# Kernel optimization log

Measured on AMD Instinct MI355X. Metric: run time of the kernel, lower is better.

## Reference

```python
import jax, jax.numpy as jnp
import numpy as np

B, C, HZ, HX = 32, 256, 13, 25

# ---------- basic layers ----------

def _conv1x1(x, w, b):
    # x: [B,Cin,H,W], w: [Cout,Cin]
    return jnp.einsum('bchw,oc->bohw', x, w) + b[None, :, None, None]

def _conv2d(x, w, b, pad):
    y = jax.lax.conv_general_dilated(x, w, (1, 1), [(pad, pad), (pad, pad)],
                                     dimension_numbers=('NCHW', 'OIHW', 'NCHW'))
    return y + b[None, :, None, None]

def _bn(x, gamma, beta, mean, var):
    # eval-mode batchnorm with running stats, eps=1e-5 (torch default)
    s = gamma / jnp.sqrt(var + 1e-5)
    return x * s[None, :, None, None] + (beta - mean * s)[None, :, None, None]

def _gelu(x):
    return jax.nn.gelu(x, approximate=False)  # torch nn.GELU default = exact erf

# ---------- sparsemax (softThresholdingOperation) ----------
# The torch topk version recursively refines unresolved rows with 2*topk; since
# 2*128>=169 and 2*512>=625 it is mathematically exact sparsemax here.

def _sparsemax_impl(s):
    s = s - jnp.max(s, axis=-1, keepdims=True)
    d = s.shape[-1]
    z = -jnp.sort(-s, axis=-1)                      # descending sort
    cs = jnp.cumsum(z, axis=-1) - 1.0
    k = jnp.arange(1, d + 1, dtype=s.dtype)
    support = k * z > cs
    supp = jnp.sum(support, axis=-1, keepdims=True)  # int support size
    tau = jnp.take_along_axis(cs, supp - 1, axis=-1) / supp.astype(s.dtype)
    out = jnp.maximum(s - tau, 0.0)
    return out, (out, supp)

@jax.custom_vjp
def sparsemax(s):
    return _sparsemax_impl(s)[0]

def _sm_fwd(s):
    return _sparsemax_impl(s)

def _sm_bwd(res, g):
    out, supp = res
    gi = jnp.where(out != 0, g, 0.0)
    v_hat = jnp.sum(gi, axis=-1, keepdims=True) / supp.astype(out.dtype)
    return (jnp.where(out != 0, gi - v_hat, gi),)

sparsemax.defvjp(_sm_fwd, _sm_bwd)

# ---------- connected components + fill holes (GPU-native, no scipy) ----------

def _dilate8_max(lab):
    # 3x3 max-pool label propagation (8-connectivity, matches np.ones((3,3)))
    Bb, H, W = lab.shape
    p = jnp.pad(lab, ((0, 0), (1, 1), (1, 1)))
    shifts = [p[:, i:i + H, j:j + W] for i in range(3) for j in range(3)]
    return jnp.max(jnp.stack(shifts, 0), 0)

def _dilate4_or(x):
    # cross-shaped binary dilation (4-connectivity, scipy fill_holes default)
    Bb, H, W = x.shape
    p = jnp.pad(x, ((0, 0), (1, 1), (1, 1)))
    return (p[:, 1:H + 1, 1:W + 1] | p[:, 0:H, 1:W + 1] | p[:, 2:H + 2, 1:W + 1]
            | p[:, 1:H + 1, 0:W] | p[:, 1:H + 1, 2:W + 2])

def _largest_cc_filled(m):
    # m: bool [B,H,W] -> float mask of largest 8-connected component, holes filled
    Bb, H, W = m.shape
    HW = H * W
    idx = jnp.arange(1, HW + 1, dtype=jnp.int32).reshape(1, H, W)
    lab0 = jnp.where(m, idx, 0)

    def body(st):
        lab, _ = st
        return (jnp.where(m, _dilate8_max(lab), 0), lab)

    lab = jax.lax.while_loop(lambda st: jnp.any(st[0] != st[1]), body,
                             (lab0, -jnp.ones_like(lab0)))[0]

    counts = jax.vmap(lambda l, mm: jnp.zeros(HW + 1, jnp.int32)
                      .at[l.ravel()].add(mm.ravel()))(lab, m.astype(jnp.int32))
    largest = jnp.argmax(counts.at[:, 0].set(-1), axis=-1).astype(jnp.int32)
    comp = (lab == largest[:, None, None]) & m

    # fill holes: flood-fill background (4-conn) from the border, invert
    bg = ~comp
    border = jnp.zeros((H, W), bool).at[0].set(True).at[-1].set(True) \
        .at[:, 0].set(True).at[:, -1].set(True)
    seed = bg & border[None]

    def body2(st):
        r, _ = st
        return (bg & _dilate4_or(r), r)

    reach = jax.lax.while_loop(lambda st: jnp.any(st[0] != st[1]), body2,
                               (seed, jnp.zeros_like(seed)))[0]
    return ~reach

# ---------- module forward ----------

def _forward(zf, xf, sup_w, sup_b, sup_gamma, sup_beta, sup_mean, sup_var,
             q_w, q_b, q_gamma, q_beta, q_mean, q_var,
             g_w1, g_b1, g_w2, g_b2, g_gamma, g_beta, g_mean, g_var,
             fi_w, fi_b, fi_gamma, fi_beta, fi_mean, fi_var,
             fi1_w, fi1_b, fi1_gamma, fi1_beta, fi1_mean, fi1_var):
    Bb, Cc, Hz, Wz = zf.shape
    _, _, Hx, Wx = xf.shape

    xf_trans = _gelu(_bn(_conv1x1(xf, q_w, q_b), q_gamma, q_beta, q_mean, q_var))
    zf_trans = _gelu(_bn(_conv1x1(zf, sup_w, sup_b), sup_gamma, sup_beta, sup_mean, sup_var))
    xf_g = _gelu(_bn(_conv1x1(_conv2d(xf, g_w1, g_b1, 1), g_w2, g_b2),
                     g_gamma, g_beta, g_mean, g_var))

    zt = zf_trans.reshape(Bb, Cc, Hz * Wz)
    xt = xf_trans.reshape(Bb, Cc, Hx * Wx)
    zp = zf.reshape(Bb, Cc, Hz * Wz)
    xp = xf.reshape(Bb, Cc, Hx * Wx)

    zf_s = sparsemax(jnp.einsum('bcn,bcm->bnm', zt, zt))      # [B,169,169]
    zp = zp + jnp.einsum('bcn,bnm->bcm', zp, zf_s)

    si = sparsemax(jnp.einsum('bcn,bcm->bnm', zp, xp))         # [B,169,625]
    si2 = sparsemax(jnp.einsum('bcn,bcm->bnm', zp, xt))
    si = si + si2

    mask2 = jax.lax.stop_gradient(jnp.mean(si2, axis=1)) != 0  # [B,625]
    mask = _largest_cc_filled(mask2.reshape(Bb, Hx, Wx)).astype(xf.dtype)[:, None]

    si_img = si.reshape(Bb, Hz * Wz, Hx, Wx)                   # [B,169,25,25]
    fi_out = _gelu(_bn(_conv1x1(si_img, fi_w, fi_b), fi_gamma, fi_beta, fi_mean, fi_var))
    concat = jnp.concatenate([fi_out, xf_g * mask], axis=1)
    return _gelu(_bn(_conv2d(concat, fi1_w, fi1_b, 2),
                     fi1_gamma, fi1_beta, fi1_mean, fi1_var))

# ---------- setup ----------

def setup_inputs() -> dict:
    key = jax.random.key(0)
    ks = jax.random.split(key, 40)
    f32 = jnp.float32

    def n(k, shape, s=0.05):
        return (jax.random.normal(k, shape) * s).astype(f32)

    inp = {}
    inp['zf'] = jax.random.normal(ks[0], (B, C, HZ, HZ), f32)
    inp['xf'] = jax.random.normal(ks[1], (B, C, HX, HX), f32)

    def bn_params(pfx, k0):
        inp[pfx + '_gamma'] = (1.0 + n(ks[k0], (C,))).astype(f32)
        inp[pfx + '_beta'] = n(ks[k0 + 1], (C,))
        inp[pfx + '_mean'] = n(ks[k0 + 2], (C,))
        inp[pfx + '_var'] = jax.random.uniform(ks[k0 + 3], (C,), f32, 0.5, 1.5)

    inp['sup_w'] = n(ks[2], (C, C), 0.06); inp['sup_b'] = n(ks[3], (C,))
    bn_params('sup', 4)
    inp['q_w'] = n(ks[8], (C, C), 0.06); inp['q_b'] = n(ks[9], (C,))
    bn_params('q', 10)
    inp['g_w1'] = n(ks[14], (C, C, 3, 3), 0.02); inp['g_b1'] = n(ks[15], (C,))
    inp['g_w2'] = n(ks[16], (C, C), 0.06); inp['g_b2'] = n(ks[17], (C,))
    bn_params('g', 18)
    inp['fi_w'] = n(ks[22], (C, HZ * HZ), 0.08); inp['fi_b'] = n(ks[23], (C,))
    bn_params('fi', 24)
    inp['fi1_w'] = n(ks[28], (C, 2 * C, 5, 5), 0.01); inp['fi1_b'] = n(ks[29], (C,))
    bn_params('fi1', 30)
    return inp


def reference(zf, xf, sup_w, sup_b, sup_gamma, sup_beta, sup_mean, sup_var,
              q_w, q_b, q_gamma, q_beta, q_mean, q_var,
              g_w1, g_b1, g_w2, g_b2, g_gamma, g_beta, g_mean, g_var,
              fi_w, fi_b, fi_gamma, fi_beta, fi_mean, fi_var,
              fi1_w, fi1_b, fi1_gamma, fi1_beta, fi1_mean, fi1_var):
    return _forward(zf, xf, sup_w, sup_b, sup_gamma, sup_beta, sup_mean, sup_var,
                    q_w, q_b, q_gamma, q_beta, q_mean, q_var,
                    g_w1, g_b1, g_w2, g_b2, g_gamma, g_beta, g_mean, g_var,
                    fi_w, fi_b, fi_gamma, fi_beta, fi_mean, fi_var,
                    fi1_w, fi1_b, fi1_gamma, fi1_beta, fi1_mean, fi1_var)
```

## Files before the change

kernel.cpp:

```cpp
#include <hip/hip_runtime.h>
#include <hip/hip_bf16.h>
#include <math.h>

#define BB  32
#define CC  256
#define NZ  169
#define NX  625

typedef _Float16 f16x4 __attribute__((ext_vector_type(4)));
typedef _Float16 f16x8 __attribute__((ext_vector_type(8)));
typedef float    f32x4 __attribute__((ext_vector_type(4)));

__device__ __forceinline__ float geluf(float x) {
  return 0.5f * x * (1.0f + erff(x * 0.7071067811865476f));
}

struct GP {
  const float* A;  const float* B;
  const float* bias; const float* gamma; const float* beta; const float* mean; const float* var;
  const float* resid;
  float* out;
  int M, N, K;
  long aB, bB, outB;
};

#define TM 64
#define TN 64
#define TK 16

template<int AG, int EPI>
__global__ __launch_bounds__(256) void gemm_k(GP p) {
  const int b  = blockIdx.z;
  const int m0 = blockIdx.y * TM;
  const int n0 = blockIdx.x * TN;
  const float* Ab = p.A + (size_t)b * p.aB;
  const float* Bb = p.B + (size_t)b * p.bB;
  __shared__ __align__(16) float As[TK][TM + 4];
  __shared__ __align__(16) float Bs[TK][TN + 4];
  const int tid = threadIdx.x;
  const int tx = tid & 15, ty = tid >> 4;
  float acc[4][4] = {{0.f}};
  const int nK = (p.K + TK - 1) / TK;
  for (int kb = 0; kb < nK; ++kb) {
    const int k0 = kb * TK;
    if (AG == 0) {
      #pragma unroll
      for (int i = 0; i < 4; ++i) {
        int e = tid * 4 + i;
        int am = e >> 4, ak = e & 15;
        int gm = m0 + am, gk = k0 + ak;
        float v = 0.f;
        if (gm < p.M && gk < p.K) v = Ab[(size_t)gm * p.K + gk];
        As[ak][am] = v;
      }
    } else {
      #pragma unroll
      for (int i = 0; i < 4; ++i) {
        int e = tid + 256 * i;
        int ak = e >> 6, am = e & 63;
        int gm = m0 + am, gk = k0 + ak;
        float v = 0.f;
        if (gm < p.M && gk < p.K) v = Ab[(size_t)gk * p.M + gm];
        As[ak][am] = v;
      }
    }
    #pragma unroll
    for (int i = 0; i < 4; ++i) {
      int e = tid + 256 * i;
      int bk = e >> 6, bn = e & 63;
      int gk = k0 + bk, gn = n0 + bn;
      float v = 0.f;
      if (gk < p.K && gn < p.N) v = Bb[(size_t)gk * p.N + gn];
      Bs[bk][bn] = v;
    }
    __syncthreads();
    #pragma unroll
    for (int kk = 0; kk < TK; ++kk) {
      float av[4], bv[4];
      #pragma unroll
      for (int i2 = 0; i2 < 4; ++i2) av[i2] = As[kk][ty * 4 + i2];
      #pragma unroll
      for (int j2 = 0; j2 < 4; ++j2) bv[j2] = Bs[kk][tx * 4 + j2];
      #pragma unroll
      for (int i2 = 0; i2 < 4; ++i2)
        #pragma unroll
        for (int j2 = 0; j2 < 4; ++j2)
          acc[i2][j2] = fmaf(av[i2], bv[j2], acc[i2][j2]);
    }
    __syncthreads();
  }
  #pragma unroll
  for (int i = 0; i < 4; ++i) {
    int gm = m0 + ty * 4 + i;
    if (gm >= p.M) continue;
    float bs = 0.f, sBN = 1.f, tBN = 0.f;
    if (EPI == 2) {
      bs = p.bias[gm];
      float sc = p.gamma[gm] / sqrtf(p.var[gm] + 1e-5f);
      sBN = sc; tBN = p.beta[gm] - p.mean[gm] * sc;
    }
    #pragma unroll
    for (int j = 0; j < 4; ++j) {
      int gn = n0 + tx * 4 + j;
      if (gn >= p.N) continue;
      float v = acc[i][j];
      if (EPI == 2) { v += bs; v = v * sBN + tBN; v = geluf(v); }
      if (EPI == 3) v += p.resid[(size_t)b * p.outB + (size_t)gm * p.N + gn];
      p.out[(size_t)b * p.outB + (size_t)gm * p.N + gn] = v;
    }
  }
}

struct GP2 {
  const float* A; const float* B1; const float* B2;
  float* out1; float* out2;
  int M, N, K;
  long aB, bB, outB;
};

__global__ __launch_bounds__(256) void gemm2_k(GP2 p) {
  const int b  = blockIdx.z;
  const int m0 = blockIdx.y * TM;
  const int n0 = blockIdx.x * TN;
  const float* Ab  = p.A  + (size_t)b * p.aB;
  const float* B1b = p.B1 + (size_t)b * p.bB;
  const float* B2b = p.B2 + (size_t)b * p.bB;
  __shared__ __align__(16) float As [TK][TM + 4];
  __shared__ __align__(16) float Bs1[TK][TN + 4];
  __shared__ __align__(16) float Bs2[TK][TN + 4];
  const int tid = threadIdx.x;
  const int tx = tid & 15, ty = tid >> 4;
  float acc1[4][4] = {{0.f}};
  float acc2[4][4] = {{0.f}};
  const int nK = (p.K + TK - 1) / TK;
  for (int kb = 0; kb < nK; ++kb) {
    const int k0 = kb * TK;
    #pragma unroll
    for (int i = 0; i < 4; ++i) {
      int e = tid + 256 * i;
      int ak = e >> 6, am = e & 63;
      int gm = m0 + am, gk = k0 + ak;
      float v = 0.f;
      if (gm < p.M && gk < p.K) v = Ab[(size_t)gk * p.M + gm];
      As[ak][am] = v;
    }
    #pragma unroll
    for (int i = 0; i < 4; ++i) {
      int e = tid + 256 * i;
      int bk = e >> 6, bn = e & 63;
      int gk = k0 + bk, gn = n0 + bn;
      float v1 = 0.f, v2 = 0.f;
      if (gk < p.K && gn < p.N) {
        v1 = B1b[(size_t)gk * p.N + gn];
        v2 = B2b[(size_t)gk * p.N + gn];
      }
      Bs1[bk][bn] = v1;
      Bs2[bk][bn] = v2;
    }
    __syncthreads();
    #pragma unroll
    for (int kk = 0; kk < TK; ++kk) {
      float av[4], bv1[4], bv2[4];
      #pragma unroll
      for (int i2 = 0; i2 < 4; ++i2) av[i2] = As[kk][ty * 4 + i2];
      #pragma unroll
      for (int j2 = 0; j2 < 4; ++j2) { bv1[j2] = Bs1[kk][tx * 4 + j2]; bv2[j2] = Bs2[kk][tx * 4 + j2]; }
      #pragma unroll
      for (int i2 = 0; i2 < 4; ++i2)
        #pragma unroll
        for (int j2 = 0; j2 < 4; ++j2) {
          acc1[i2][j2] = fmaf(av[i2], bv1[j2], acc1[i2][j2]);
          acc2[i2][j2] = fmaf(av[i2], bv2[j2], acc2[i2][j2]);
        }
    }
    __syncthreads();
  }
  #pragma unroll
  for (int i = 0; i < 4; ++i) {
    int gm = m0 + ty * 4 + i;
    if (gm >= p.M) continue;
    #pragma unroll
    for (int j = 0; j < 4; ++j) {
      int gn = n0 + tx * 4 + j;
      if (gn >= p.N) continue;
      size_t o = (size_t)b * p.outB + (size_t)gm * p.N + gn;
      p.out1[o] = acc1[i][j];
      p.out2[o] = acc2[i][j];
    }
  }
}

__global__ __launch_bounds__(256) void wtr_k(const float* __restrict__ W,
                                             _Float16* __restrict__ Wt,
                                             int M, int C2, int C2p, int R) {
  size_t o = (size_t)blockIdx.x * 256 + threadIdx.x;
  size_t total = (size_t)R * M * C2p;
  if (o >= total) return;
  int c = (int)(o % C2p);
  int t = (int)(o / C2p);
  int m = t % M;
  int r = t / M;
  float v = 0.f;
  if (c < C2) v = W[((size_t)m * C2 + c) * R + r];
  Wt[o] = (_Float16)v;
}

__global__ __launch_bounds__(256) void cvt_k(const float* __restrict__ A,
                                             const float* __restrict__ A2,
                                             _Float16* __restrict__ O,
                                             int C, int Cp, long total) {
  long o = (long)blockIdx.x * 256 + threadIdx.x;
  if (o >= total) return;
  int c = (int)(o % Cp);
  long t = o / Cp;
  int pp = (int)(t % NX);
  int b = (int)(t / NX);
  float v = 0.f;
  if (c < C) {
    size_t src = ((size_t)b * C + c) * NX + pp;
    v = A[src];
    if (A2) v += A2[src];
  }
  O[o] = (_Float16)v;
}

struct MP {
  const _Float16* Wt;
  const _Float16* U;
  const float* mask;
  const float* bias; const float* gamma; const float* beta; const float* mean; const float* var;
  float* out;
  _Float16* out16;
  int R, Rw, C2p;
  long uB;
  int oC2p, oCoff;
};

template<int EPI, int OUT16, int MASKED>
__global__ __launch_bounds__(256) void mgemm_k(MP p) {
  const int L   = blockIdx.x + 10 * (blockIdx.y + 4 * blockIdx.z);
  const int xcd = L & 7;
  const int j   = L >> 3;
  const int jb  = j / 40;
  const int b   = (xcd << 2) + jb;
  const int t   = j - jb * 40;
  const int m0  = (t / 10) * 64;
  const int n0  = (t - (t / 10) * 10) * 64;

  __shared__ __align__(16) _Float16 As[64][64];
  __shared__ __align__(16) _Float16 Bs[64][64];
  const int tid = threadIdx.x;
  const int w = tid >> 6, lane = tid & 63;
  const int wm = w & 1, wn = w >> 1;
  const int lm = lane & 15, q = lane >> 4;
  const int sr = tid >> 2, sc4 = tid & 3;
  const int scc = sc4 * 16;
  const int sr7 = sr & 7, sb = sc4 * 2;
  const int ng = n0 + sr;
  const bool nv = ng < NX;
  const int py = ng / 25, px = ng - (ng / 25) * 25;
  const _Float16* Ub = p.U + (size_t)b * p.uB;
  const float* mb = MASKED ? (p.mask + (size_t)b * NX) : nullptr;
  const int pad = p.Rw >> 1;

  f32x4 acc[2][2] = {};

  for (int r = 0; r < p.R; ++r) {
    const int kh = r / p.Rw, kw = r - (r / p.Rw) * p.Rw;
    const int iy = py + kh - pad, ix = px + kw - pad;
    const bool pv = nv && ((unsigned)iy < 25u) && ((unsigned)ix < 25u);
    const int pp = iy * 25 + ix;
    const _Float16* Up = pv ? (Ub + (size_t)pp * p.C2p) : nullptr;
    _Float16 mh = (_Float16)1.f;
    if (MASKED && pv) mh = (_Float16)mb[pp];
    const _Float16* Wr = p.Wt + ((size_t)r * 256 + m0) * p.C2p;
    for (int c0 = 0; c0 < p.C2p; c0 += 64) {
      const _Float16* Arow = Wr + (size_t)sr * p.C2p + c0 + scc;
      f16x8 a0 = *(const f16x8*)(Arow);
      f16x8 a1 = *(const f16x8*)(Arow + 8);
      f16x8 v0 = {}, v1 = {};
      if (pv) {
        const _Float16* Bp = Up + c0 + scc;
        v0 = *(const f16x8*)(Bp);
        v1 = *(const f16x8*)(Bp + 8);
        if (MASKED && (c0 + scc) >= 256) { v0 = v0 * mh; v1 = v1 * mh; }
      }
      *(f16x8*)&As[sr][((sb + 0) ^ sr7) << 3] = a0;
      *(f16x8*)&As[sr][((sb + 1) ^ sr7) << 3] = a1;
      *(f16x8*)&Bs[sr][((sb + 0) ^ sr7) << 3] = v0;
      *(f16x8*)&Bs[sr][((sb + 1) ^ sr7) << 3] = v1;
      __syncthreads();
      #pragma unroll
      for (int ks = 0; ks < 2; ++ks) {
        const int so = (((ks << 2) + q) ^ (lm & 7)) << 3;
        f16x8 af[2], bf[2];
        #pragma unroll
        for (int fm = 0; fm < 2; ++fm)
          af[fm] = *(const f16x8*)&As[wm * 32 + fm * 16 + lm][so];
        #pragma unroll
        for (int fn = 0; fn < 2; ++fn)
          bf[fn] = *(const f16x8*)&Bs[wn * 32 + fn * 16 + lm][so];
        #pragma unroll
        for (int fm = 0; fm < 2; ++fm)
          #pragma unroll
          for (int fn = 0; fn < 2; ++fn)
            acc[fm][fn] = __builtin_amdgcn_mfma_f32_16x16x32_f16(
                af[fm], bf[fn], acc[fm][fn], 0, 0, 0);
      }
      __syncthreads();
    }
  }
  #pragma unroll
  for (int fm = 0; fm < 2; ++fm) {
    const int rbase = m0 + wm * 32 + fm * 16 + q * 4;
    #pragma unroll
    for (int rr = 0; rr < 4; ++rr) {
      const int row = rbase + rr;
      float bs = p.bias[row];
      float sBN = 1.f, tBN = 0.f;
      if (EPI == 2) {
        float sc = p.gamma[row] / sqrtf(p.var[row] + 1e-5f);
        sBN = sc; tBN = p.beta[row] - p.mean[row] * sc;
      }
      #pragma unroll
      for (int fn = 0; fn < 2; ++fn) {
        const int col = n0 + wn * 32 + fn * 16 + lm;
        if (col < NX) {
          float v = acc[fm][fn][rr] + bs;
          if (EPI == 2) v = geluf(v * sBN + tBN);
          if (OUT16) {
            p.out16[((size_t)b * NX + col) * p.oC2p + p.oCoff + row] = (_Float16)v;
          } else {
            p.out[(size_t)b * (256 * NX) + (size_t)row * NX + col] = v;
          }
        }
      }
    }
  }
}

__global__ __launch_bounds__(256) void sparsemax_k(float* __restrict__ S, int d) {
  const int row = blockIdx.x;
  float* s = S + (size_t)row * d;
  const int tid = threadIdx.x;
  const int wid = tid >> 6, lane = tid & 63;
  float v[3]; bool act[3];
  #pragma unroll
  for (int j = 0; j < 3; ++j) {
    int idx = tid + j * 256;
    bool ok = idx < d;
    v[j] = ok ? s[idx] : -1e30f;
    act[j] = ok;
  }
  __shared__ float red[16];
  float mx = fmaxf(fmaxf(v[0], v[1]), v[2]);
  #pragma unroll
  for (int o = 32; o; o >>= 1) mx = fmaxf(mx, __shfl_down(mx, o));
  if (lane == 0) red[wid] = mx;
  __syncthreads();
  if (tid == 0) red[0] = fmaxf(fmaxf(red[0], red[1]), fmaxf(red[2], red[3]));
  __syncthreads();
  mx = red[0];
  __syncthreads();
  #pragma unroll
  for (int j = 0; j < 3; ++j) if (act[j]) v[j] -= mx;
  float tau = 0.f;
  for (int it = 0; it < 700; ++it) {
    float ls = 0.f, lc = 0.f;
    #pragma unroll
    for (int j = 0; j < 3; ++j) if (act[j]) { ls += v[j]; lc += 1.f; }
    #pragma unroll
    for (int o = 32; o; o >>= 1) { ls += __shfl_down(ls, o); lc += __shfl_down(lc, o); }
    if (lane == 0) { red[wid] = ls; red[4 + wid] = lc; }
    __syncthreads();
    if (tid == 0) {
      float Sm = 0.f, Cn = 0.f;
      #pragma unroll
      for (int w2 = 0; w2 < 4; ++w2) { Sm += red[w2]; Cn += red[4 + w2]; }
      red[8] = (Sm - 1.f) / Cn;
      red[9] = 0.f;
    }
    __syncthreads();
    tau = red[8];
    bool ch = false;
    #pragma unroll
    for (int j = 0; j < 3; ++j)
      if (act[j] && v[j] <= tau) { act[j] = false; ch = true; }
    if (ch) red[9] = 1.f;
    __syncthreads();
    if (red[9] == 0.f) break;
  }
  #pragma unroll
  for (int j = 0; j < 3; ++j) {
    int idx = tid + j * 256;
    if (idx < d) s[idx] = fmaxf(v[j] - tau, 0.f);
  }
}

__global__ __launch_bounds__(640) void cc_kernel(const float* __restrict__ si2,
                                                 float* __restrict__ mask) {
  const int b = blockIdx.x, tid = threadIdx.x;
  __shared__ int lab[625];
  __shared__ int counts[626];
  __shared__ int flag, best;
  const bool in = tid < 625;
  const int y = tid / 25, x = tid - (tid / 25) * 25;
  bool mv = false;
  if (in) {
    const float* base = si2 + (size_t)b * NZ * NX + tid;
    for (int n = 0; n < NZ; ++n) mv = mv || (base[(size_t)n * NX] > 0.f);
    lab[tid] = mv ? tid + 1 : 0;
  }
  __syncthreads();
  for (int it = 0; it < 1000; ++it) {
    if (tid == 0) flag = 0;
    __syncthreads();
    int nl = 0;
    if (in && mv) {
      nl = lab[tid];
      #pragma unroll
      for (int dy = -1; dy <= 1; ++dy)
        #pragma unroll
        for (int dx = -1; dx <= 1; ++dx) {
          int yy = y + dy, xx = x + dx;
          if ((unsigned)yy < 25u && (unsigned)xx < 25u) nl = max(nl, lab[yy * 25 + xx]);
        }
    }
    __syncthreads();
    if (in && mv && nl != lab[tid]) { lab[tid] = nl; flag = 1; }
    __syncthreads();
    if (flag == 0) break;
  }
  if (tid < 626) counts[tid] = (tid == 0) ? -1 : 0;
  if (tid == 0) best = (int)0x80000000;
  __syncthreads();
  if (in && mv) atomicAdd(&counts[lab[tid]], 1);
  __syncthreads();
  if (tid < 626) atomicMax(&best, counts[tid] * 1024 + (1023 - tid));
  __syncthreads();
  const int largest = 1023 - (best & 1023);
  const bool comp = in && mv && (lab[tid] == largest);
  const bool bg = in && !comp;
  const bool border = in && (y == 0 || y == 24 || x == 0 || x == 24);
  __syncthreads();
  if (in) lab[tid] = (bg && border) ? 1 : 0;
  __syncthreads();
  for (int it = 0; it < 1000; ++it) {
    if (tid == 0) flag = 0;
    __syncthreads();
    int r = 0;
    if (in && bg && !lab[tid]) {
      if (y > 0  && lab[tid - 25]) r = 1;
      if (y < 24 && lab[tid + 25]) r = 1;
      if (x > 0  && lab[tid - 1])  r = 1;
      if (x < 24 && lab[tid + 1])  r = 1;
    }
    __syncthreads();
    if (r) { lab[tid] = 1; flag = 1; }
    __syncthreads();
    if (flag == 0) break;
  }
  if (in) mask[(size_t)b * NX + tid] = lab[tid] ? 0.f : 1.f;
}

extern "C" void kernel_launch(void* const* d_in, const int* in_sizes, int n_in,
                              void* d_out, int out_size, void* d_ws, size_t ws_size,
                              hipStream_t stream) {
  const float* zf     = (const float*)d_in[0];
  const float* xf     = (const float*)d_in[1];
  const float* sup_w  = (const float*)d_in[2];
  const float* sup_b  = (const float*)d_in[3];
  const float* sup_g  = (const float*)d_in[4];
  const float* sup_be = (const float*)d_in[5];
  const float* sup_m  = (const float*)d_in[6];
  const float* sup_v  = (const float*)d_in[7];
  const float* q_w    = (const float*)d_in[8];
  const float* q_b    = (const float*)d_in[9];
  const float* q_g    = (const float*)d_in[10];
  const float* q_be   = (const float*)d_in[11];
  const float* q_m    = (const float*)d_in[12];
  const float* q_v    = (const float*)d_in[13];
  const float* g_w1   = (const float*)d_in[14];
  const float* g_b1   = (const float*)d_in[15];
  const float* g_w2   = (const float*)d_in[16];
  const float* g_b2   = (const float*)d_in[17];
  const float* g_g    = (const float*)d_in[18];
  const float* g_be   = (const float*)d_in[19];
  const float* g_m    = (const float*)d_in[20];
  const float* g_v    = (const float*)d_in[21];
  const float* fi_w   = (const float*)d_in[22];
  const float* fi_b   = (const float*)d_in[23];
  const float* fi_g   = (const float*)d_in[24];
  const float* fi_be  = (const float*)d_in[25];
  const float* fi_m   = (const float*)d_in[26];
  const float* fi_v   = (const float*)d_in[27];
  const float* fi1_w  = (const float*)d_in[28];
  const float* fi1_b  = (const float*)d_in[29];
  const float* fi1_g  = (const float*)d_in[30];
  const float* fi1_be = (const float*)d_in[31];
  const float* fi1_m  = (const float*)d_in[32];
  const float* fi1_v  = (const float*)d_in[33];

  float* ws = (float*)d_ws;
  float* xf_trans = ws;
  float* zf_trans = xf_trans + 5120000;
  float* zf_s     = zf_trans + 1384448;
  float* zp2      = zf_s + 913952;
  float* si       = zp2 + 1384448;
  float* si2      = si + 3380000;
  float* maskb    = si2 + 3380000;
  float* tail     = maskb + 20000;

  _Float16* xf16 = (_Float16*)tail;
  _Float16* gt16 = xf16 + 5120000;
  _Float16* Ucat = gt16 + 5120000;
  _Float16* S16  = Ucat + 10240000;

  _Float16* wt_g1  = (_Float16*)xf_trans;
  _Float16* wt_g2  = wt_g1 + 589824;
  _Float16* wt_fi  = wt_g2 + 65536;
  _Float16* wt_fi1 = wt_fi + 49152;

  dim3 blk(256);
  GP p;

  p = GP{}; p.A = q_w; p.B = xf; p.bias = q_b;
  p.gamma = q_g; p.beta = q_be; p.mean = q_m; p.var = q_v;
  p.out = xf_trans; p.M = CC; p.N = NX; p.K = CC;
  p.aB = 0; p.bB = (long)CC * NX; p.outB = (long)CC * NX;
  gemm_k<0,2><<<dim3(10,4,BB), blk, 0, stream>>>(p);

  p = GP{}; p.A = sup_w; p.B = zf; p.bias = sup_b;
  p.gamma = sup_g; p.beta = sup_be; p.mean = sup_m; p.var = sup_v;
  p.out = zf_trans; p.M = CC; p.N = NZ; p.K = CC;
  p.aB = 0; p.bB = (long)CC * NZ; p.outB = (long)CC * NZ;
  gemm_k<0,2><<<dim3(3,4,BB), blk, 0, stream>>>(p);

  p = GP{}; p.A = zf_trans; p.B = zf_trans;
  p.out = zf_s; p.M = NZ; p.N = NZ; p.K = CC;
  p.aB = (long)CC * NZ; p.bB = (long)CC * NZ; p.outB = (long)NZ * NZ;
  gemm_k<1,0><<<dim3(3,3,BB), blk, 0, stream>>>(p);

  sparsemax_k<<<BB * NZ, blk, 0, stream>>>(zf_s, NZ);

  p = GP{}; p.A = zf; p.B = zf_s; p.resid = zf;
  p.out = zp2; p.M = CC; p.N = NZ; p.K = NZ;
  p.aB = (long)CC * NZ; p.bB = (long)NZ * NZ; p.outB = (long)CC * NZ;
  gemm_k<0,3><<<dim3(3,4,BB), blk, 0, stream>>>(p);

  {
    GP2 p2{};
    p2.A = zp2; p2.B1 = xf; p2.B2 = xf_trans;
    p2.out1 = si; p2.out2 = si2;
    p2.M = NZ; p2.N = NX; p2.K = CC;
    p2.aB = (long)CC * NZ; p2.bB = (long)CC * NX; p2.outB = (long)NZ * NX;
    gemm2_k<<<dim3(10,3,BB), blk, 0, stream>>>(p2);
  }

  sparsemax_k<<<2 * BB * NZ, blk, 0, stream>>>(si, NX);

  cc_kernel<<<BB, dim3(640), 0, stream>>>(si2, maskb);

  wtr_k<<<(9*256*256 + 255)/256,  blk, 0, stream>>>(g_w1,  wt_g1,  256, 256, 256, 9);
  wtr_k<<<(256*256   + 255)/256,  blk, 0, stream>>>(g_w2,  wt_g2,  256, 256, 256, 1);
  wtr_k<<<(256*192   + 255)/256,  blk, 0, stream>>>(fi_w,  wt_fi,  256, 169, 192, 1);
  wtr_k<<<(25*256*512+ 255)/256,  blk, 0, stream>>>(fi1_w, wt_fi1, 256, 512, 512, 25);

  cvt_k<<<(long)(BB*NX*256 + 255)/256, blk, 0, stream>>>(xf, nullptr, xf16, 256, 256, (long)BB*NX*256);
  cvt_k<<<(long)(BB*NX*192 + 255)/256, blk, 0, stream>>>(si, si2, S16, 169, 192, (long)BB*NX*192);

  MP mp;

  mp = MP{}; mp.Wt = wt_g1; mp.U = xf16; mp.bias = g_b1;
  mp.out16 = gt16; mp.R = 9; mp.Rw = 3; mp.C2p = 256;
  mp.uB = (long)NX * 256; mp.oC2p = 256; mp.oCoff = 0;
  mgemm_k<1,1,0><<<dim3(10,4,BB), blk, 0, stream>>>(mp);

  mp = MP{}; mp.Wt = wt_g2; mp.U = gt16; mp.bias = g_b2;
  mp.gamma = g_g; mp.beta = g_be; mp.mean = g_m; mp.var = g_v;
  mp.out16 = Ucat; mp.R = 1; mp.Rw = 1; mp.C2p = 256;
  mp.uB = (long)NX * 256; mp.oC2p = 512; mp.oCoff = 256;
  mgemm_k<2,1,0><<<dim3(10,4,BB), blk, 0, stream>>>(mp);

  mp = MP{}; mp.Wt = wt_fi; mp.U = S16; mp.bias = fi_b;
  mp.gamma = fi_g; mp.beta = fi_be; mp.mean = fi_m; mp.var = fi_v;
  mp.out16 = Ucat; mp.R = 1; mp.Rw = 1; mp.C2p = 192;
  mp.uB = (long)NX * 192; mp.oC2p = 512; mp.oCoff = 0;
  mgemm_k<2,1,0><<<dim3(10,4,BB), blk, 0, stream>>>(mp);

  mp = MP{}; mp.Wt = wt_fi1; mp.U = Ucat; mp.mask = maskb;
  mp.bias = fi1_b; mp.gamma = fi1_g; mp.beta = fi1_be; mp.mean = fi1_m; mp.var = fi1_v;
  mp.out = (float*)d_out; mp.R = 25; mp.Rw = 5; mp.C2p = 512;
  mp.uB = (long)NX * 512;
  mgemm_k<2,0,1><<<dim3(10,4,BB), blk, 0, stream>>>(mp);
}
```

Baseline: 833.9 us.

## Map each sparsemax row to one wavefront instead of one block

Measured after the change: 783.4 us (median of 2 runs). 1.06x faster.

```diff
diff --git a/kernel.cpp b/kernel.cpp
--- a/kernel.cpp
+++ b/kernel.cpp
@@ -339,60 +339,47 @@
   }
 }
 
-__global__ __launch_bounds__(256) void sparsemax_k(float* __restrict__ S, int d) {
-  const int row = blockIdx.x;
+template<int NE>
+__global__ __launch_bounds__(256) void sparsemax_w(float* __restrict__ S,
+                                                   int d, int nrows) {
+  const int row = blockIdx.x * 4 + (threadIdx.x >> 6);
+  const int lane = threadIdx.x & 63;
+  if (row >= nrows) return;
   float* s = S + (size_t)row * d;
-  const int tid = threadIdx.x;
-  const int wid = tid >> 6, lane = tid & 63;
-  float v[3]; bool act[3];
-  #pragma unroll
-  for (int j = 0; j < 3; ++j) {
-    int idx = tid + j * 256;
+  float v[NE]; bool act[NE];
+  #pragma unroll
+  for (int j = 0; j < NE; ++j) {
+    int idx = lane + 64 * j;
     bool ok = idx < d;
+    act[j] = ok;
     v[j] = ok ? s[idx] : -1e30f;
-    act[j] = ok;
-  }
-  __shared__ float red[16];
-  float mx = fmaxf(fmaxf(v[0], v[1]), v[2]);
+  }
+  float mx = v[0];
+  #pragma unroll
+  for (int j = 1; j < NE; ++j) mx = fmaxf(mx, v[j]);
   #pragma unroll
   for (int o = 32; o; o >>= 1) mx = fmaxf(mx, __shfl_down(mx, o));
-  if (lane == 0) red[wid] = mx;
-  __syncthreads();
-  if (tid == 0) red[0] = fmaxf(fmaxf(red[0], red[1]), fmaxf(red[2], red[3]));
-  __syncthreads();
-  mx = red[0];
-  __syncthreads();
-  #pragma unroll
-  for (int j = 0; j < 3; ++j) if (act[j]) v[j] -= mx;
+  mx = __shfl(mx, 0);
+  #pragma unroll
+  for (int j = 0; j < NE; ++j) if (act[j]) v[j] -= mx;
   float tau = 0.f;
   for (int it = 0; it < 700; ++it) {
     float ls = 0.f, lc = 0.f;
     #pragma unroll
-    for (int j = 0; j < 3; ++j) if (act[j]) { ls += v[j]; lc += 1.f; }
+    for (int j = 0; j < NE; ++j) if (act[j]) { ls += v[j]; lc += 1.f; }
     #pragma unroll
     for (int o = 32; o; o >>= 1) { ls += __shfl_down(ls, o); lc += __shfl_down(lc, o); }
-    if (lane == 0) { red[wid] = ls; red[4 + wid] = lc; }
-    __syncthreads();
-    if (tid == 0) {
-      float Sm = 0.f, Cn = 0.f;
-      #pragma unroll
-      for (int w2 = 0; w2 < 4; ++w2) { Sm += red[w2]; Cn += red[4 + w2]; }
-      red[8] = (Sm - 1.f) / Cn;
-      red[9] = 0.f;
-    }
-    __syncthreads();
-    tau = red[8];
+    ls = __shfl(ls, 0); lc = __shfl(lc, 0);
+    tau = (ls - 1.f) / lc;
     bool ch = false;
     #pragma unroll
-    for (int j = 0; j < 3; ++j)
+    for (int j = 0; j < NE; ++j)
       if (act[j] && v[j] <= tau) { act[j] = false; ch = true; }
-    if (ch) red[9] = 1.f;
-    __syncthreads();
-    if (red[9] == 0.f) break;
-  }
-  #pragma unroll
-  for (int j = 0; j < 3; ++j) {
-    int idx = tid + j * 256;
+    if (!__any(ch)) break;
+  }
+  #pragma unroll
+  for (int j = 0; j < NE; ++j) {
+    int idx = lane + 64 * j;
     if (idx < d) s[idx] = fmaxf(v[j] - tau, 0.f);
   }
 }
@@ -541,7 +528,7 @@
   p.aB = (long)CC * NZ; p.bB = (long)CC * NZ; p.outB = (long)NZ * NZ;
   gemm_k<1,0><<<dim3(3,3,BB), blk, 0, stream>>>(p);
 
-  sparsemax_k<<<BB * NZ, blk, 0, stream>>>(zf_s, NZ);
+  sparsemax_w<3><<<(BB * NZ + 3) / 4, blk, 0, stream>>>(zf_s, NZ, BB * NZ);
 
   p = GP{}; p.A = zf; p.B = zf_s; p.resid = zf;
   p.out = zp2; p.M = CC; p.N = NZ; p.K = NZ;
@@ -557,7 +544,7 @@
     gemm2_k<<<dim3(10,3,BB), blk, 0, stream>>>(p2);
   }
 
-  sparsemax_k<<<2 * BB * NZ, blk, 0, stream>>>(si, NX);
+  sparsemax_w<10><<<(2 * BB * NZ + 3) / 4, blk, 0, stream>>>(si, NX, 2 * BB * NZ);
 
   cc_kernel<<<BB, dim3(640), 0, stream>>>(si2, maskb);
 
```
